# Optimization experiments

Hardware: AMD Instinct MI355X
Metric: run time of the kernel (lower is better)

Reference implementation:

```python
import jax, jax.numpy as jnp
import numpy as np
import math

E = 4096  # embed_dim
H = 32    # num_heads
M = 256   # max_queries
B = 8     # batch
N = 256   # kv tokens (16x16 grid -> no pos-embed interpolation branch)


def _sincos_1d(d, pos):
    omega = np.arange(d // 2, dtype=np.float32) / (d / 2.0)
    omega = 1.0 / 10000 ** omega
    out = np.einsum('m,d->md', pos.reshape(-1), omega)
    return np.concatenate([np.sin(out), np.cos(out)], axis=1)


def _sincos_2d(embed_dim, grid_size):
    gh = np.arange(grid_size, dtype=np.float32)
    gw = np.arange(grid_size, dtype=np.float32)
    grid = np.stack(np.meshgrid(gw, gh), axis=0).reshape(2, -1)
    return np.concatenate([
        _sincos_1d(embed_dim // 2, grid[0]),
        _sincos_1d(embed_dim // 2, grid[1]),
    ], axis=1)


def setup_inputs() -> dict:
    key = jax.random.key(0)
    ks = jax.random.split(key, 4)
    grid_size = int(math.ceil(math.sqrt(M)))
    pe = _sincos_2d(E, grid_size)[:M].astype(np.float32)
    return {
        'x': jax.random.normal(ks[0], (B, N, E), jnp.float32),
        'query': 0.02 * jax.random.normal(ks[1], (M, E), jnp.float32),
        'pos_embed': jnp.asarray(pe),
        'ln_q_w': jnp.ones((E,), jnp.float32),
        'ln_q_b': jnp.zeros((E,), jnp.float32),
        'ln_kv_w': jnp.ones((E,), jnp.float32),
        'ln_kv_b': jnp.zeros((E,), jnp.float32),
        'in_proj_w': 0.02 * jax.random.normal(ks[2], (3 * E, E), jnp.float32),
        'in_proj_b': jnp.zeros((3 * E,), jnp.float32),
        'out_proj_w': 0.02 * jax.random.normal(ks[3], (E, E), jnp.float32),
        'out_proj_b': jnp.zeros((E,), jnp.float32),
    }


def _ln(x, w, b, eps=1e-5):
    m = jnp.mean(x, -1, keepdims=True)
    v = jnp.mean((x - m) ** 2, -1, keepdims=True)
    return (x - m) * jax.lax.rsqrt(v + eps) * w + b


def reference(x, query, pos_embed, ln_q_w, ln_q_b, ln_kv_w, ln_kv_b,
              in_proj_w, in_proj_b, out_proj_w, out_proj_b):
    D = E // H
    kv = _ln(x, ln_kv_w, ln_kv_b)                      # [B,N,E] (kv_proj is Identity)
    q_in = _ln(query, ln_q_w, ln_q_b) + pos_embed      # [M,E] (Q + posQ, shared over batch)
    k_in = kv + pos_embed[None]                        # N == M so posK == pos_embed (no interp)
    Wq, Wk, Wv = in_proj_w[:E], in_proj_w[E:2 * E], in_proj_w[2 * E:]
    bq, bk, bv = in_proj_b[:E], in_proj_b[E:2 * E], in_proj_b[2 * E:]
    q = (q_in @ Wq.T + bq).reshape(M, H, D).transpose(1, 0, 2)          # [H,M,D]
    k = (k_in @ Wk.T + bk).reshape(B, N, H, D).transpose(0, 2, 1, 3)    # [B,H,N,D]
    v = (kv @ Wv.T + bv).reshape(B, N, H, D).transpose(0, 2, 1, 3)      # [B,H,N,D]
    scores = jnp.einsum('hmd,bhnd->bhmn', q, k) / jnp.sqrt(jnp.float32(D))
    attn = jax.nn.softmax(scores, axis=-1)                              # [B,H,M,N]
    o = jnp.einsum('bhmn,bhnd->bhmd', attn, v)
    o = o.transpose(0, 2, 1, 3).reshape(B, M, E)
    out = o @ out_proj_w.T + out_proj_b                                 # [B,M,E]
    # need_weights=True with average_attn_weights=True -> head-averaged weights
    return out, attn.mean(axis=1)
```

## Files before the change

kernel.cpp:

```cpp
#include <hip/hip_runtime.h>
#include <hip/hip_bf16.h>

typedef __bf16 bf16;
typedef __attribute__((ext_vector_type(8))) __bf16 bf16x8;
typedef __attribute__((ext_vector_type(4))) __bf16 bf16x4;
typedef __attribute__((ext_vector_type(4))) float floatx4;

#define E_DIM 4096
#define H_DIM 32
#define D_DIM 128
#define M_DIM 256
#define B_DIM 8
#define N_DIM 256

#define GLD_LDS(g, l) __builtin_amdgcn_global_load_lds( \
    (const __attribute__((address_space(1))) unsigned int*)(g), \
    (__attribute__((address_space(3))) unsigned int*)(l), 16, 0, 0)

__device__ __forceinline__ float wave_sum(float v) {
#pragma unroll
  for (int o = 32; o; o >>= 1) v += __shfl_xor(v, o);
  return v;
}
__device__ __forceinline__ float wave_max(float v) {
#pragma unroll
  for (int o = 32; o; o >>= 1) v = fmaxf(v, __shfl_xor(v, o));
  return v;
}

#define BAR256() asm volatile("s_barrier" ::: "memory")
#define LGKM0_256()                                      \
  asm volatile("s_waitcnt lgkmcnt(0)" ::: "memory");     \
  __builtin_amdgcn_sched_barrier(0)

#define STAGE_A256(T, h)                                                       \
  {                                                                            \
    _Pragma("unroll") for (int j = 0; j < 2; ++j)                              \
        GLD_LDS(Ag + (size_t)((h)*128 + sgrow + j * 8) * lda + (T) * 64 + sgcol, \
                AsP + ((T)&1) * 16384 + (h)*8192 + sdst + j * 512);            \
  }
#define STAGE_B256(T, h)                                                       \
  {                                                                            \
    _Pragma("unroll") for (int j = 0; j < 2; ++j)                              \
        GLD_LDS(Bg + (size_t)((h)*128 + sgrow + j * 8) * ldb + (T) * 64 + sgcol, \
                BsP + ((T)&1) * 16384 + (h)*8192 + sdst + j * 512);            \
  }
#define LDA256(mh)                                                             \
  {                                                                            \
    _Pragma("unroll") for (int m = 0; m < 4; ++m) {                            \
      a[m][0] = *(const bf16x8*)(AsP + buf + rA + ((mh)*4 + m) * 1024 + slot0); \
      a[m][1] = *(const bf16x8*)(AsP + buf + rA + ((mh)*4 + m) * 1024 + slot1); \
    }                                                                          \
  }
#define LDB256(dst, nh)                                                        \
  {                                                                            \
    _Pragma("unroll") for (int n = 0; n < 2; ++n) {                            \
      dst[n][0] = *(const bf16x8*)(BsP + buf + rB + ((nh)*2 + n) * 1024 + slot0); \
      dst[n][1] = *(const bf16x8*)(BsP + buf + rB + ((nh)*2 + n) * 1024 + slot1); \
    }                                                                          \
  }
#define MFMAQ(mb, nb, B)                                                       \
  {                                                                            \
    _Pragma("unroll") for (int m = 0; m < 4; ++m)                              \
        _Pragma("unroll") for (int n = 0; n < 2; ++n) {                        \
      acc[(mb) + m][(nb) + n] = __builtin_amdgcn_mfma_f32_16x16x32_bf16(       \
          a[m][0], B[n][0], acc[(mb) + m][(nb) + n], 0, 0, 0);                 \
      acc[(mb) + m][(nb) + n] = __builtin_amdgcn_mfma_f32_16x16x32_bf16(       \
          a[m][1], B[n][1], acc[(mb) + m][(nb) + n], 0, 0, 0);                 \
    }                                                                          \
  }

__device__ __forceinline__ void gemm256_core(const bf16* __restrict__ Ag,
                                             const bf16* __restrict__ Bg,
                                             int lda, int ldb, int nkt,
                                             bf16* AsP, bf16* BsP,
                                             floatx4 (&acc)[8][4],
                                             int wid, int lane) {
  const int wm = wid >> 2, wn = wid & 3;
  const int l15 = lane & 15, q = lane >> 4, e7 = lane & 7;
  const int slot0 = ((q ^ e7) & 7) * 8;
  const int slot1 = (((4 + q) ^ e7) & 7) * 8;
  const int rA = (wm * 128 + l15) * 64;
  const int rB = (wn * 64 + l15) * 64;
  const int sgrow = wid * 16 + (lane >> 3);
  const int sgcol = ((lane & 7) ^ (lane >> 3)) * 8;
  const int sdst = wid * 1024;

  bf16x8 a[4][2], b0[2][2], b1[2][2];

  STAGE_B256(0, 0); STAGE_B256(0, 1);
  STAGE_A256(0, 0); STAGE_A256(0, 1);
  STAGE_B256(1, 0); STAGE_B256(1, 1);

  for (int U = 0; U < nkt; ++U) {
    const int buf = (U & 1) * 16384;
    if (U + 1 < nkt)
      asm volatile("s_waitcnt vmcnt(4)\n\ts_barrier" ::: "memory");
    else
      asm volatile("s_waitcnt vmcnt(0)\n\ts_barrier" ::: "memory");
    LDA256(0); LDB256(b0, 0);
    if (U + 1 < nkt) { STAGE_A256(U + 1, 0); }
    BAR256(); LGKM0_256();
    __builtin_amdgcn_s_setprio(1); MFMAQ(0, 0, b0); __builtin_amdgcn_s_setprio(0);
    __builtin_amdgcn_sched_barrier(0); BAR256();
    LDB256(b1, 1);
    if (U + 1 < nkt) { STAGE_A256(U + 1, 1); }
    BAR256(); LGKM0_256();
    __builtin_amdgcn_s_setprio(1); MFMAQ(0, 2, b1); __builtin_amdgcn_s_setprio(0);
    __builtin_amdgcn_sched_barrier(0); BAR256();
    LDA256(1);
    if (U + 2 < nkt) { STAGE_B256(U + 2, 0); }
    BAR256(); LGKM0_256();
    __builtin_amdgcn_s_setprio(1); MFMAQ(4, 2, b1); __builtin_amdgcn_s_setprio(0);
    __builtin_amdgcn_sched_barrier(0); BAR256();
    if (U + 2 < nkt) { STAGE_B256(U + 2, 1); }
    BAR256();
    __builtin_amdgcn_s_setprio(1); MFMAQ(4, 0, b0); __builtin_amdgcn_s_setprio(0);
    __builtin_amdgcn_sched_barrier(0);
  }
}

__global__ __launch_bounds__(512, 1)
void proj256(const bf16* __restrict__ qin, const bf16* __restrict__ kin,
             const bf16* __restrict__ kv, const bf16* __restrict__ Wqkv,
             const float* __restrict__ bqkv, bf16* __restrict__ qp,
             bf16* __restrict__ kp, bf16* __restrict__ vt) {
  __shared__ __align__(16) bf16 As2[32768];
  __shared__ __align__(16) bf16 Bs2[32768];
  const int tid = threadIdx.x, wid = tid >> 6, lane = tid & 63;

  const int o = blockIdx.x;
  const int id = (o & 7) * 34 + (o >> 3);
  int role, bx, by;
  const bf16 *A, *B;
  const float* bias;
  bf16* C;
  if (id < 128) {
    role = 1; by = id & 7; bx = id >> 3;
    A = kin; B = Wqkv + 16777216; bias = bqkv + 4096; C = kp;
  } else if (id < 256) {
    role = 2; by = (id - 128) & 7; bx = (id - 128) >> 3;
    A = kv; B = Wqkv + 33554432; bias = bqkv + 8192; C = vt;
  } else {
    role = 0; by = 0; bx = id - 256;
    A = qin; B = Wqkv; bias = bqkv; C = qp;
  }
  const int trowA = by * 256, trowB = bx * 256;
  const bf16* Ag = A + (size_t)trowA * E_DIM;
  const bf16* Bg = B + (size_t)trowB * E_DIM;

  floatx4 acc[8][4];
#pragma unroll
  for (int i = 0; i < 8; ++i)
#pragma unroll
    for (int j = 0; j < 4; ++j) acc[i][j] = (floatx4){0.f, 0.f, 0.f, 0.f};

  gemm256_core(Ag, Bg, E_DIM, E_DIM, 64, As2, Bs2, acc, wid, lane);

  const int wm = wid >> 2, wn = wid & 3;
  const int l15 = lane & 15, q = lane >> 4;
  const int mrow0 = trowA + wm * 128 + q * 4;
  const int ncol0 = trowB + wn * 64 + l15;
  if (role != 2) {
#pragma unroll
    for (int m = 0; m < 8; ++m)
#pragma unroll
      for (int n = 0; n < 4; ++n) {
        const int col = ncol0 + n * 16;
        const float bb = bias[col];
        floatx4 v = acc[m][n];
#pragma unroll
        for (int r = 0; r < 4; ++r)
          C[(size_t)(mrow0 + m * 16 + r) * E_DIM + col] = (bf16)(v[r] + bb);
      }
  } else {
#pragma unroll
    for (int m = 0; m < 8; ++m)
#pragma unroll
      for (int n = 0; n < 4; ++n) {
        const int col = ncol0 + n * 16;
        const int h = col >> 7, d = col & 127;
        const float bb = bias[col];
        const int row0 = mrow0 + m * 16;
        const int b_ = row0 >> 8, n_ = row0 & 255;
        floatx4 v = acc[m][n];
        bf16x4 p;
#pragma unroll
        for (int r = 0; r < 4; ++r) p[r] = (bf16)(v[r] + bb);
        *(bf16x4*)(C + ((size_t)((b_ * H_DIM + h) * D_DIM + d)) * N_DIM + n_) = p;
      }
  }
}

__global__ __launch_bounds__(512, 1)
void outproj256(const bf16* __restrict__ obuf, const bf16* __restrict__ Wout,
                float* __restrict__ Cf) {
  __shared__ __align__(16) bf16 As2[32768];
  __shared__ __align__(16) bf16 Bs2[32768];
  const int tid = threadIdx.x, wid = tid >> 6, lane = tid & 63;

  const int o = blockIdx.x;
  const int id = (o & 7) * 32 + (o >> 3);
  const int z = id >> 7;
  const int t = id & 127;
  const int by = t & 7, bx = t >> 3;
  const int trowA = by * 256, trowB = bx * 256;
  const bf16* Ag = obuf + (size_t)z * 2048 + (size_t)trowA * E_DIM;
  const bf16* Bg = Wout + (size_t)z * 2048 + (size_t)trowB * E_DIM;

  floatx4 acc[8][4];
#pragma unroll
  for (int i = 0; i < 8; ++i)
#pragma unroll
    for (int j = 0; j < 4; ++j) acc[i][j] = (floatx4){0.f, 0.f, 0.f, 0.f};

  gemm256_core(Ag, Bg, E_DIM, E_DIM, 32, As2, Bs2, acc, wid, lane);

  const int wm = wid >> 2, wn = wid & 3;
  const int l15 = lane & 15, q = lane >> 4;
  const int mrow0 = trowA + wm * 128 + q * 4;
  const int ncol0 = trowB + wn * 64 + l15;
#pragma unroll
  for (int m = 0; m < 8; ++m)
#pragma unroll
    for (int n = 0; n < 4; ++n) {
      const int col = ncol0 + n * 16;
      floatx4 v = acc[m][n];
#pragma unroll
      for (int r = 0; r < 4; ++r)
        Cf[(size_t)z * 8388608 + (size_t)(mrow0 + m * 16 + r) * E_DIM + col] = v[r];
    }
}

__device__ __forceinline__ void gemm_core_small(const bf16* __restrict__ Arow,
                                                const bf16* __restrict__ Brow,
                                                int lda, int ldb, int kTiles,
                                                bf16* As, bf16* Bs,
                                                floatx4 (&acc)[4][4],
                                                int wid, int lane) {
  const int s0 = wid * 2;
  const int lp = lane ^ ((lane >> 3) & 7);
  const int srow = lp >> 2;
  const int skoff = (lp & 3) * 8;
  const int rA = (wid >> 1) * 64 + (lane & 15);
  const int rB = (wid & 1) * 64 + (lane & 15);
  const int q16 = (lane >> 4) * 8;
  const int ex = (((lane & 15) >> 1) & 7) << 3;

#pragma unroll
  for (int c = 0; c < 2; ++c) {
    const int s = s0 + c;
    const int row = s * 16 + srow;
    GLD_LDS(Arow + (size_t)row * lda + skoff, As + s * 512);
    GLD_LDS(Brow + (size_t)row * ldb + skoff, Bs + s * 512);
  }

  for (int kt = 0; kt < kTiles; ++kt) {
    const int cur = (kt & 1) * 4096;
    const int nxt = 4096 - cur;
    __syncthreads();
    if (kt + 1 < kTiles) {
      const int k0 = (kt + 1) << 5;
#pragma unroll
      for (int c = 0; c < 2; ++c) {
        const int s = s0 + c;
        const int row = s * 16 + srow;
        GLD_LDS(Arow + (size_t)row * lda + k0 + skoff, As + nxt + s * 512);
        GLD_LDS(Brow + (size_t)row * ldb + k0 + skoff, Bs + nxt + s * 512);
      }
    }
    bf16x8 af[4], bfr[4];
#pragma unroll
    for (int t = 0; t < 4; ++t) {
      af[t] = *(const bf16x8*)(As + cur + ((((rA + t * 16) * 32) + q16) ^ ex));
      bfr[t] = *(const bf16x8*)(Bs + cur + ((((rB + t * 16) * 32) + q16) ^ ex));
    }
#pragma unroll
    for (int tr = 0; tr < 4; ++tr)
#pragma unroll
      for (int tc = 0; tc < 4; ++tc)
        acc[tr][tc] = __builtin_amdgcn_mfma_f32_16x16x32_bf16(af[tr], bfr[tc],
                                                              acc[tr][tc], 0, 0, 0);
  }
}

__global__ __launch_bounds__(256) void cvt_all_kernel(const float* __restrict__ s1,
                                                      bf16* __restrict__ d1,
                                                      const float* __restrict__ s2,
                                                      bf16* __restrict__ d2) {
  long i = ((long)blockIdx.x * 256 + threadIdx.x) * 8;
  const float* src;
  bf16* dst;
  if (i < 50331648L) { src = s1 + i; dst = d1 + i; }
  else { src = s2 + (i - 50331648L); dst = d2 + (i - 50331648L); }
  float4 a = *(const float4*)(src);
  float4 b = *(const float4*)(src + 4);
  bf16x8 p;
  p[0] = (bf16)a.x; p[1] = (bf16)a.y; p[2] = (bf16)a.z; p[3] = (bf16)a.w;
  p[4] = (bf16)b.x; p[5] = (bf16)b.y; p[6] = (bf16)b.z; p[7] = (bf16)b.w;
  *(bf16x8*)(dst) = p;
}

__global__ __launch_bounds__(256) void ln_x_kernel(const float* __restrict__ x,
                                                   const float* __restrict__ w,
                                                   const float* __restrict__ bvec,
                                                   const float* __restrict__ pos,
                                                   bf16* __restrict__ kv,
                                                   bf16* __restrict__ kin) {
  const int row = blockIdx.x;
  const int n = row & (N_DIM - 1);
  const int tid = threadIdx.x, wid = tid >> 6, lane = tid & 63;
  const float* xr = x + (size_t)row * E_DIM;
  float4 v[4];
  float s1 = 0.f, s2 = 0.f;
#pragma unroll
  for (int j = 0; j < 4; ++j) {
    v[j] = *(const float4*)(xr + j * 1024 + tid * 4);
    s1 += v[j].x + v[j].y + v[j].z + v[j].w;
    s2 += v[j].x * v[j].x + v[j].y * v[j].y + v[j].z * v[j].z + v[j].w * v[j].w;
  }
  s1 = wave_sum(s1); s2 = wave_sum(s2);
  __shared__ float red[8];
  if (lane == 0) { red[wid] = s1; red[wid + 4] = s2; }
  __syncthreads();
  s1 = red[0] + red[1] + red[2] + red[3];
  s2 = red[4] + red[5] + red[6] + red[7];
  const float mean = s1 * (1.f / E_DIM);
  const float var = s2 * (1.f / E_DIM) - mean * mean;
  const float rs = rsqrtf(var + 1e-5f);
#pragma unroll
  for (int j = 0; j < 4; ++j) {
    const int idx = j * 1024 + tid * 4;
    float4 wv = *(const float4*)(w + idx);
    float4 bv = *(const float4*)(bvec + idx);
    float4 pv = *(const float4*)(pos + (size_t)n * E_DIM + idx);
    float y0 = (v[j].x - mean) * rs * wv.x + bv.x;
    float y1 = (v[j].y - mean) * rs * wv.y + bv.y;
    float y2 = (v[j].z - mean) * rs * wv.z + bv.z;
    float y3 = (v[j].w - mean) * rs * wv.w + bv.w;
    bf16x4 a; a[0] = (bf16)y0; a[1] = (bf16)y1; a[2] = (bf16)y2; a[3] = (bf16)y3;
    *(bf16x4*)(kv + (size_t)row * E_DIM + idx) = a;
    bf16x4 c; c[0] = (bf16)(y0 + pv.x); c[1] = (bf16)(y1 + pv.y);
    c[2] = (bf16)(y2 + pv.z); c[3] = (bf16)(y3 + pv.w);
    *(bf16x4*)(kin + (size_t)row * E_DIM + idx) = c;
  }
}

__global__ __launch_bounds__(256) void ln_q_kernel(const float* __restrict__ q,
                                                   const float* __restrict__ w,
                                                   const float* __restrict__ bvec,
                                                   const float* __restrict__ pos,
                                                   bf16* __restrict__ qin) {
  const int row = blockIdx.x;
  const int tid = threadIdx.x, wid = tid >> 6, lane = tid & 63;
  const float* xr = q + (size_t)row * E_DIM;
  float4 v[4];
  float s1 = 0.f, s2 = 0.f;
#pragma unroll
  for (int j = 0; j < 4; ++j) {
    v[j] = *(const float4*)(xr + j * 1024 + tid * 4);
    s1 += v[j].x + v[j].y + v[j].z + v[j].w;
    s2 += v[j].x * v[j].x + v[j].y * v[j].y + v[j].z * v[j].z + v[j].w * v[j].w;
  }
  s1 = wave_sum(s1); s2 = wave_sum(s2);
  __shared__ float red[8];
  if (lane == 0) { red[wid] = s1; red[wid + 4] = s2; }
  __syncthreads();
  s1 = red[0] + red[1] + red[2] + red[3];
  s2 = red[4] + red[5] + red[6] + red[7];
  const float mean = s1 * (1.f / E_DIM);
  const float var = s2 * (1.f / E_DIM) - mean * mean;
  const float rs = rsqrtf(var + 1e-5f);
#pragma unroll
  for (int j = 0; j < 4; ++j) {
    const int idx = j * 1024 + tid * 4;
    float4 wv = *(const float4*)(w + idx);
    float4 bv = *(const float4*)(bvec + idx);
    float4 pv = *(const float4*)(pos + (size_t)row * E_DIM + idx);
    bf16x4 a;
    a[0] = (bf16)((v[j].x - mean) * rs * wv.x + bv.x + pv.x);
    a[1] = (bf16)((v[j].y - mean) * rs * wv.y + bv.y + pv.y);
    a[2] = (bf16)((v[j].z - mean) * rs * wv.z + bv.z + pv.z);
    a[3] = (bf16)((v[j].w - mean) * rs * wv.w + bv.w + pv.w);
    *(bf16x4*)(qin + (size_t)row * E_DIM + idx) = a;
  }
}

template <int MODE>
__global__ __launch_bounds__(256, 2)
void gemm_bt(const bf16* __restrict__ Abase, const bf16* __restrict__ Bbase,
             float* __restrict__ Cf, bf16* __restrict__ Cb,
             int K, int lda, int ldb, int ldc, float scale) {
  __shared__ __align__(16) bf16 As[8192];
  __shared__ __align__(16) bf16 Bs[8192];
  const int tid = threadIdx.x;
  const int wid = tid >> 6;
  const int lane = tid & 63;

  const bf16* A = Abase;
  const bf16* B = Bbase;
  if constexpr (MODE == 2) {
    int z = blockIdx.z; int zb = z >> 5, zh = z & 31;
    A += zh * D_DIM;
    B += ((size_t)zb * N_DIM) * E_DIM + zh * D_DIM;
  } else if constexpr (MODE == 3) {
    int z = blockIdx.z;
    A += (size_t)z * M_DIM * 512;
    B += (size_t)z * D_DIM * N_DIM;
  }

  const bf16* Arow = A + (size_t)(blockIdx.y * 128) * lda;
  const bf16* Brow = B + (size_t)(blockIdx.x * 128) * ldb;

  floatx4 acc[4][4];
#pragma unroll
  for (int i = 0; i < 4; ++i)
#pragma unroll
    for (int j = 0; j < 4; ++j) acc[i][j] = (floatx4){0.f, 0.f, 0.f, 0.f};

  gemm_core_small(Arow, Brow, lda, ldb, K >> 5, As, Bs, acc, wid, lane);

  const int mb = blockIdx.y * 128 + (wid >> 1) * 64 + (lane >> 4) * 4;
  const int nb = blockIdx.x * 128 + (wid & 1) * 64 + (lane & 15);
#pragma unroll
  for (int tr = 0; tr < 4; ++tr) {
#pragma unroll
    for (int tc = 0; tc < 4; ++tc) {
      const int row0 = mb + tr * 16;
      const int col = nb + tc * 16;
      floatx4 a = acc[tr][tc];
      if constexpr (MODE == 2) {
#pragma unroll
        for (int r = 0; r < 4; ++r)
          Cf[(size_t)blockIdx.z * (M_DIM * N_DIM) + (size_t)(row0 + r) * ldc + col] =
              a[r] * scale;
      } else {
        int z = blockIdx.z; int zb_ = z >> 5, zh_ = z & 31;
#pragma unroll
        for (int r = 0; r < 4; ++r)
          Cb[(size_t)zb_ * M_DIM * E_DIM + (size_t)(row0 + r) * E_DIM + zh_ * D_DIM + col] =
              (bf16)a[r];
      }
    }
  }
}

__global__ __launch_bounds__(256) void reduce_out_kernel(const float* __restrict__ p,
                                                         const float* __restrict__ bias,
                                                         float* __restrict__ out) {
  const size_t i = ((size_t)blockIdx.x * 256 + threadIdx.x) * 4;
  float4 a = *(const float4*)(p + i);
  float4 b = *(const float4*)(p + 8388608 + i);
  float4 bb = *(const float4*)(bias + (i & 4095));
  float4 o;
  o.x = a.x + b.x + bb.x; o.y = a.y + b.y + bb.y;
  o.z = a.z + b.z + bb.z; o.w = a.w + b.w + bb.w;
  *(float4*)(out + i) = o;
}

__global__ __launch_bounds__(256) void softmax_mean_kernel(float* __restrict__ scores,
                                                           float* __restrict__ out_mean) {
  const int bm = blockIdx.x;
  const int b = bm >> 8, m = bm & 255;
  const int wid = threadIdx.x >> 6, lane = threadIdx.x & 63;
  float a0 = 0.f, a1 = 0.f, a2 = 0.f, a3 = 0.f;
  for (int j = 0; j < 8; ++j) {
    const int h = wid * 8 + j;
    float* row = scores + ((size_t)((b * H_DIM + h) * M_DIM + m)) * N_DIM;
    float4 v = *(const float4*)(row + lane * 4);
    float mx = fmaxf(fmaxf(v.x, v.y), fmaxf(v.z, v.w));
    mx = wave_max(mx);
    v.x = __expf(v.x - mx); v.y = __expf(v.y - mx);
    v.z = __expf(v.z - mx); v.w = __expf(v.w - mx);
    const float s = wave_sum(v.x + v.y + v.z + v.w);
    const float inv = 1.f / s;
    v.x *= inv; v.y *= inv; v.z *= inv; v.w *= inv;
    a0 += v.x; a1 += v.y; a2 += v.z; a3 += v.w;
    bf16x4 p; p[0] = (bf16)v.x; p[1] = (bf16)v.y; p[2] = (bf16)v.z; p[3] = (bf16)v.w;
    *(bf16x4*)((bf16*)row + lane * 4) = p;
  }
  __shared__ float red[4][256];
  *(float4*)&red[wid][lane * 4] = make_float4(a0, a1, a2, a3);
  __syncthreads();
  if (wid == 0) {
    float4 r0 = *(float4*)&red[0][lane * 4];
    float4 r1 = *(float4*)&red[1][lane * 4];
    float4 r2 = *(float4*)&red[2][lane * 4];
    float4 r3 = *(float4*)&red[3][lane * 4];
    float4 o;
    o.x = (r0.x + r1.x + r2.x + r3.x) * (1.f / H_DIM);
    o.y = (r0.y + r1.y + r2.y + r3.y) * (1.f / H_DIM);
    o.z = (r0.z + r1.z + r2.z + r3.z) * (1.f / H_DIM);
    o.w = (r0.w + r1.w + r2.w + r3.w) * (1.f / H_DIM);
    *(float4*)(out_mean + (size_t)bm * N_DIM + lane * 4) = o;
  }
}

extern "C" void kernel_launch(void* const* d_in, const int* in_sizes, int n_in,
                              void* d_out, int out_size, void* d_ws, size_t ws_size,
                              hipStream_t stream) {
  const float* x = (const float*)d_in[0];
  const float* query = (const float*)d_in[1];
  const float* pos = (const float*)d_in[2];
  const float* ln_q_w = (const float*)d_in[3];
  const float* ln_q_b = (const float*)d_in[4];
  const float* ln_kv_w = (const float*)d_in[5];
  const float* ln_kv_b = (const float*)d_in[6];
  const float* Wqkv_f = (const float*)d_in[7];
  const float* bqkv = (const float*)d_in[8];
  const float* Wout_f = (const float*)d_in[9];
  const float* bout = (const float*)d_in[10];

  char* ws = (char*)d_ws;
  bf16* Wqkv = (bf16*)(ws + 0);
  bf16* Wout = (bf16*)(ws + 100663296);
  bf16* kv   = (bf16*)(ws + 134217728);
  bf16* kin  = (bf16*)(ws + 150994944);
  bf16* qin  = (bf16*)(ws + 167772160);
  bf16* qp   = (bf16*)(ws + 169869312);
  bf16* kp   = (bf16*)(ws + 171966464);
  bf16* vt   = (bf16*)(ws + 188743680);
  float* partials = (float*)(ws + 205520896);
  float* scores = (float*)(ws + 0);
  bf16* obuf = (bf16*)(ws + 67108864);

  float* out = (float*)d_out;
  float* out2 = out + (size_t)B_DIM * M_DIM * E_DIM;

  cvt_all_kernel<<<32768, 256, 0, stream>>>(Wqkv_f, Wqkv, Wout_f, Wout);
  ln_x_kernel<<<2048, 256, 0, stream>>>(x, ln_kv_w, ln_kv_b, pos, kv, kin);
  ln_q_kernel<<<256, 256, 0, stream>>>(query, ln_q_w, ln_q_b, pos, qin);

  proj256<<<272, 512, 0, stream>>>(qin, kin, kv, Wqkv, bqkv, qp, kp, vt);

  gemm_bt<2><<<dim3(2, 2, 256), 256, 0, stream>>>(qp, kp, scores, nullptr,
                                                  128, 4096, 4096, 256,
                                                  0.08838834764831845f);
  softmax_mean_kernel<<<2048, 256, 0, stream>>>(scores, out2);
  gemm_bt<3><<<dim3(1, 2, 256), 256, 0, stream>>>((const bf16*)scores, vt,
                                                  nullptr, obuf,
                                                  256, 512, 256, 4096, 1.f);
  outproj256<<<256, 512, 0, stream>>>(obuf, Wout, partials);
  reduce_out_kernel<<<8192, 256, 0, stream>>>(partials, bout, out);
}
```

Before: 827.6 us.

## Split Q projection into split-K chunks appended to K/V projection blocks

The Q projection previously ran as 16 extra 256x256 tiles with full K=4096, creating a tail wave of 272 blocks on 256 CUs. Now each of the 256 K/V blocks also computes a 256-wide K-chunk of one Q tile and writes fp32 partials, and a new reduce kernel sums the 16 partials, adds the bias and converts to bf16. This balances the work to exactly one wave, at the cost of extra fp32 partial traffic and an additional kernel launch.

```diff
diff --git a/kernel.cpp b/kernel.cpp
--- a/kernel.cpp
+++ b/kernel.cpp
@@ -123,14 +123,14 @@
 __global__ __launch_bounds__(512, 1)
 void proj256(const bf16* __restrict__ qin, const bf16* __restrict__ kin,
              const bf16* __restrict__ kv, const bf16* __restrict__ Wqkv,
-             const float* __restrict__ bqkv, bf16* __restrict__ qp,
+             const float* __restrict__ bqkv, float* __restrict__ qpart,
              bf16* __restrict__ kp, bf16* __restrict__ vt) {
   __shared__ __align__(16) bf16 As2[32768];
   __shared__ __align__(16) bf16 Bs2[32768];
   const int tid = threadIdx.x, wid = tid >> 6, lane = tid & 63;
 
   const int o = blockIdx.x;
-  const int id = (o & 7) * 34 + (o >> 3);
+  const int id = (o & 7) * 32 + (o >> 3);
   int role, bx, by;
   const bf16 *A, *B;
   const float* bias;
@@ -138,12 +138,9 @@
   if (id < 128) {
     role = 1; by = id & 7; bx = id >> 3;
     A = kin; B = Wqkv + 16777216; bias = bqkv + 4096; C = kp;
-  } else if (id < 256) {
+  } else {
     role = 2; by = (id - 128) & 7; bx = (id - 128) >> 3;
     A = kv; B = Wqkv + 33554432; bias = bqkv + 8192; C = vt;
-  } else {
-    role = 0; by = 0; bx = id - 256;
-    A = qin; B = Wqkv; bias = bqkv; C = qp;
   }
   const int trowA = by * 256, trowB = bx * 256;
   const bf16* Ag = A + (size_t)trowA * E_DIM;
@@ -161,7 +158,7 @@
   const int l15 = lane & 15, q = lane >> 4;
   const int mrow0 = trowA + wm * 128 + q * 4;
   const int ncol0 = trowB + wn * 64 + l15;
-  if (role != 2) {
+  if (role == 1) {
 #pragma unroll
     for (int m = 0; m < 8; ++m)
 #pragma unroll
@@ -190,6 +187,44 @@
         *(bf16x4*)(C + ((size_t)((b_ * H_DIM + h) * D_DIM + d)) * N_DIM + n_) = p;
       }
   }
+
+  const int qx = id & 15, kc = id >> 4;
+  const bf16* Agq = qin + kc * 256;
+  const bf16* Bgq = Wqkv + (size_t)(qx * 256) * E_DIM + kc * 256;
+#pragma unroll
+  for (int i = 0; i < 8; ++i)
+#pragma unroll
+    for (int j = 0; j < 4; ++j) acc[i][j] = (floatx4){0.f, 0.f, 0.f, 0.f};
+
+  gemm256_core(Agq, Bgq, E_DIM, E_DIM, 4, As2, Bs2, acc, wid, lane);
+
+  float* qdst = qpart + (size_t)kc * 1048576;
+  const int qmrow0 = wm * 128 + q * 4;
+  const int qncol0 = qx * 256 + wn * 64 + l15;
+#pragma unroll
+  for (int m = 0; m < 8; ++m)
+#pragma unroll
+    for (int n = 0; n < 4; ++n) {
+      const int col = qncol0 + n * 16;
+      floatx4 v = acc[m][n];
+#pragma unroll
+      for (int r = 0; r < 4; ++r)
+        qdst[(size_t)(qmrow0 + m * 16 + r) * E_DIM + col] = v[r];
+    }
+}
+
+__global__ __launch_bounds__(256) void qreduce_kernel(const float* __restrict__ qpart,
+                                                      const float* __restrict__ bias,
+                                                      bf16* __restrict__ qp) {
+  const size_t i = ((size_t)blockIdx.x * 256 + threadIdx.x) * 4;
+  float4 s = *(const float4*)(bias + (i & 4095));
+#pragma unroll
+  for (int kc = 0; kc < 16; ++kc) {
+    float4 v = *(const float4*)(qpart + (size_t)kc * 1048576 + i);
+    s.x += v.x; s.y += v.y; s.z += v.z; s.w += v.w;
+  }
+  bf16x4 p; p[0] = (bf16)s.x; p[1] = (bf16)s.y; p[2] = (bf16)s.z; p[3] = (bf16)s.w;
+  *(bf16x4*)(qp + i) = p;
 }
 
 __global__ __launch_bounds__(512, 1)
@@ -521,6 +556,7 @@
   bf16* kp   = (bf16*)(ws + 171966464);
   bf16* vt   = (bf16*)(ws + 188743680);
   float* partials = (float*)(ws + 205520896);
+  float* qpart = partials;
   float* scores = (float*)(ws + 0);
   bf16* obuf = (bf16*)(ws + 67108864);
 
@@ -531,7 +567,8 @@
   ln_x_kernel<<<2048, 256, 0, stream>>>(x, ln_kv_w, ln_kv_b, pos, kv, kin);
   ln_q_kernel<<<256, 256, 0, stream>>>(query, ln_q_w, ln_q_b, pos, qin);
 
-  proj256<<<272, 512, 0, stream>>>(qin, kin, kv, Wqkv, bqkv, qp, kp, vt);
+  proj256<<<256, 512, 0, stream>>>(qin, kin, kv, Wqkv, bqkv, qpart, kp, vt);
+  qreduce_kernel<<<1024, 256, 0, stream>>>(qpart, bqkv, qp);
 
   gemm_bt<2><<<dim3(2, 2, 256), 256, 0, stream>>>(qp, kp, scores, nullptr,
                                                   128, 4096, 4096, 256,
```

Result: faster. 732.6 us (-11.5%).
